# Performance work log

Measured on AMD Instinct MI355X. Metric: run time of the kernel, lower is better.

The kernel has to match this reference:

```python
import jax, jax.numpy as jnp
import numpy as np

T = 128        # number of time points
D = 64         # flattened state dim (bs * z_dim, bs = 1)
H = 256        # hidden width of f-network
HK = 128       # hidden width of kernel network
MAX_IT = 3     # fixed-point iterations (args.max_iterations)


def setup_inputs() -> dict:
    key = jax.random.key(0)
    ks = jax.random.split(key, 6)
    g = lambda k, sh, sc: (jax.random.normal(k, sh, jnp.float32) * sc)
    z0 = jax.random.normal(ks[0], (1, D), jnp.float32)
    t = jnp.linspace(0.0, 1.0, T, dtype=jnp.float32)
    # f: D -> H -> D MLP (the 'func' integrand network)
    W1 = g(ks[1], (D, H), 1.0 / np.sqrt(D)); b1 = jnp.zeros((H,), jnp.float32)
    W2 = g(ks[2], (H, D), 1.0 / np.sqrt(H)); b2 = jnp.zeros((D,), jnp.float32)
    # kernel: (x, s) -> D*D matrix entries (the neural kernel K)
    Wk1 = g(ks[3], (2, HK), 1.0 / np.sqrt(2.0)); bk1 = jnp.zeros((HK,), jnp.float32)
    Wk2 = g(ks[4], (HK, D * D), 1.0 / np.sqrt(HK)); bk2 = jnp.zeros((D * D,), jnp.float32)
    return dict(z0=z0, t=t, W1=W1, b1=b1, W2=W2, b2=b2,
                Wk1=Wk1, bk1=bk1, Wk2=Wk2, bk2=bk2)


def _trapezoid_weights(t):
    """w[i, j]: trapezoid quadrature weight of node j for integral over [t0, t_i]."""
    dt = t[1] - t[0]  # uniform grid
    idx = jnp.arange(T)
    mask = (idx[None, :] <= idx[:, None]).astype(t.dtype)
    w = dt * mask
    w = w.at[(idx, idx)].multiply(0.5)   # halve right endpoint of each row
    w = w.at[:, 0].multiply(0.5)         # halve left endpoint
    w = w.at[0].set(0.0)                 # zero-length integral at t0
    return w


def _solve(z0, t, W1, b1, W2, b2, Wk1, bk1, Wk2, bk2):
    y0 = z0.reshape(-1)                                   # [D], solver flattens batch
    w = _trapezoid_weights(t)                             # [T, T]
    # Neural kernel K(x_i, s_j) -> [D, D], precomputed once on the grid.
    pairs = jnp.stack([jnp.broadcast_to(t[:, None], (T, T)),
                       jnp.broadcast_to(t[None, :], (T, T))], axis=-1)  # [T, T, 2]
    hK = jnp.tanh(pairs @ Wk1 + bk1)                      # [T, T, HK]
    K = (hK @ Wk2 + bk2).reshape(T, T, D, D)              # [T, T, D, D]

    def f(y):  # integrand network, applied over all time points
        return jnp.tanh(y @ W1 + b1) @ W2 + b2            # [T, D]

    def step(y, _):
        # G_i = \int_0^{x_i} K(x_i, s) f(y(s)) ds  (trapezoid on grid)
        G = jnp.einsum('ij,ijde,je->id', w, K, f(y))      # [T, D]
        # y'(x) = G(x)  =>  y_i = y0 + \int_0^{x_i} G(s) ds
        y_new = y0[None, :] + w @ G                       # [T, D]
        return y_new, None

    y_init = jnp.tile(y0[None, :], (T, 1))                # fixed-point initial guess
    y, _ = jax.lax.scan(step, y_init, None, length=MAX_IT)
    return y


def reference(z0, t, W1, b1, W2, b2, Wk1, bk1, Wk2, bk2):
    y = _solve(z0, t, W1, b1, W2, b2, Wk1, bk1, Wk2, bk2)  # [T, D]
    return y[-1].reshape(1, D)  # z[-1]: final state, shape [bs, dim]
```

## Files before the change

kernel.cpp:

```cpp
#include <hip/hip_runtime.h>

#define TT 128
#define DD 64
#define HH 256
#define HKD 128
#define HD (HKD*DD)

static __device__ __forceinline__ float ald(const float* p) {
    return __hip_atomic_load(const_cast<float*>(p), __ATOMIC_RELAXED, __HIP_MEMORY_SCOPE_AGENT);
}
static __device__ __forceinline__ void ast(float* p, float v) {
    __hip_atomic_store(p, v, __ATOMIC_RELAXED, __HIP_MEMORY_SCOPE_AGENT);
}
static __device__ __forceinline__ int aldi(int* p) {
    return __hip_atomic_load(p, __ATOMIC_RELAXED, __HIP_MEMORY_SCOPE_AGENT);
}

__global__ void __launch_bounds__(256)
k_init(const float* __restrict__ z0, const float* __restrict__ t,
       const float* __restrict__ W1, const float* __restrict__ b1,
       const float* __restrict__ W2, const float* __restrict__ b2,
       const float* __restrict__ Wk1, const float* __restrict__ bk1,
       const float* __restrict__ Wk2, const float* __restrict__ bk2,
       float* __restrict__ M0, float* __restrict__ bF0,
       float* __restrict__ Ga, float* __restrict__ Gb, int* m0cnt)
{
    const int b = blockIdx.x, tid = threadIdx.x;
    const int part = tid >> 6, d = tid & 63;
    const float dt = t[1] - t[0];
    __shared__ float red[4][64];
    __shared__ float ys[DD];
    __shared__ float hs[HH];
    __shared__ __attribute__((aligned(16))) float fs[DD];
    __shared__ float Bpart[2][HKD];
    __shared__ float Bs[HKD];

    if (b < 32) {
        if (tid < DD) ys[tid] = z0[tid];
        __syncthreads();
        float acc = b1[tid];
        #pragma unroll 8
        for (int e = 0; e < DD; ++e) acc += ys[e] * W1[e * HH + tid];
        hs[tid] = tanhf(acc);
        __syncthreads();
        {
            float s = 0.f;
            #pragma unroll 8
            for (int h = part * 64; h < part * 64 + 64; ++h) s += hs[h] * W2[h * DD + d];
            red[part][d] = s;
        }
        __syncthreads();
        if (part == 0)
            fs[d] = b2[d] + red[0][d] + red[1][d] + red[2][d] + red[3][d];
        __syncthreads();
        if (b == 0) {
            float s = 0.f;
            #pragma unroll
            for (int e = part * 16; e < part * 16 + 16; ++e) s += bk2[d * DD + e] * fs[e];
            red[part][d] = s;
            __syncthreads();
            if (part == 0)
                ast(&bF0[d], red[0][d] + red[1][d] + red[2][d] + red[3][d]);
        }
        {
            int hd = b * 256 + tid;
            const float* Wrow = Wk2 + (size_t)hd * DD;
            float a = 0.f;
            #pragma unroll
            for (int e = 0; e < DD; e += 8) {
                float4 wa = *(const float4*)(Wrow + e);
                float4 wb = *(const float4*)(Wrow + e + 4);
                float4 fa = *(const float4*)&fs[e];
                float4 fb = *(const float4*)&fs[e + 4];
                a += fa.x*wa.x + fa.y*wa.y + fa.z*wa.z + fa.w*wa.w
                   + fb.x*wb.x + fb.y*wb.y + fb.z*wb.z + fb.w*wb.w;
            }
            ast(&M0[hd], a);
        }
        Gb[b * 256 + tid] = 0.f;
        __syncthreads();
        asm volatile("" ::: "memory");
        if (tid == 0)
            __hip_atomic_fetch_add(m0cnt, 1, __ATOMIC_RELAXED, __HIP_MEMORY_SCOPE_AGENT);
        return;
    }

    const int i = b - 32;
    {
        const int h = tid & 127, half = tid >> 7;
        float bsum = 0.f;
        if (i > 0) {
            const float wk0 = Wk1[h], wk1v = Wk1[HKD + h], bk = bk1[h];
            const float ti = t[i];
            for (int j = half; j <= i; j += 2) {
                float w = dt * ((j == 0 || j == i) ? 0.5f : 1.0f);
                bsum += w * tanhf(ti * wk0 + t[j] * wk1v + bk);
            }
        }
        Bpart[half][h] = bsum;
    }
    __syncthreads();
    if (tid < HKD) Bs[tid] = Bpart[0][tid] + Bpart[1][tid];
    if (tid == 0) { while (aldi(m0cnt) < 32) __builtin_amdgcn_s_sleep(2); }
    asm volatile("" ::: "memory");
    __syncthreads();
    float a = 0.f;
    #pragma unroll 8
    for (int h2 = part * 32; h2 < part * 32 + 32; ++h2)
        a += Bs[h2] * ald(&M0[h2 * DD + d]);
    red[part][d] = a;
    __syncthreads();
    if (part == 0) {
        float g = red[0][d] + red[1][d] + red[2][d] + red[3][d];
        g += dt * (float)i * ald(&bF0[d]);
        Ga[i * DD + d] = (i == 0) ? 0.f : g;
    }
}

__global__ void __launch_bounds__(256)
k_FM(const float* __restrict__ Gin, const float* __restrict__ z0,
     const float* __restrict__ t,
     const float* __restrict__ W1, const float* __restrict__ b1,
     const float* __restrict__ W2, const float* __restrict__ b2,
     const float* __restrict__ bk2, const float* __restrict__ Wk2,
     float* __restrict__ fbuf, float* __restrict__ bFb,
     float* __restrict__ M, int* ftile,
     float* __restrict__ out, int seed_out)
{
    const int b = blockIdx.x, tid = threadIdx.x;
    const int part = tid >> 6, d = tid & 63;
    __shared__ float red[4][64];
    __shared__ float ys[DD];
    __shared__ float hs[HH];
    __shared__ __attribute__((aligned(16))) float Fs[8][DD];
    const float dt = t[1] - t[0];

    if (b < TT) {
        const int j = b;
        float s = 0.f;
        if (j > 0) {
            for (int jp = part; jp <= j; jp += 4) {
                float w = (jp == 0 || jp == j) ? 0.5f : 1.0f;
                s += w * Gin[jp * DD + d];
            }
        }
        red[part][d] = s;
        __syncthreads();
        if (part == 0)
            ys[d] = z0[d] + dt * (red[0][d] + red[1][d] + red[2][d] + red[3][d]);
        __syncthreads();
        float acc = b1[tid];
        #pragma unroll 8
        for (int e = 0; e < DD; ++e) acc += ys[e] * W1[e * HH + tid];
        hs[tid] = tanhf(acc);
        __syncthreads();
        {
            float s2 = 0.f;
            #pragma unroll 8
            for (int h = part * 64; h < part * 64 + 64; ++h) s2 += hs[h] * W2[h * DD + d];
            red[part][d] = s2;
        }
        __syncthreads();
        if (part == 0) {
            float fv = b2[d] + red[0][d] + red[1][d] + red[2][d] + red[3][d];
            ast(&fbuf[j * DD + d], fv);
            ys[d] = fv;
        }
        __syncthreads();
        {
            float s2 = 0.f;
            #pragma unroll
            for (int e = part * 16; e < part * 16 + 16; ++e) s2 += bk2[d * DD + e] * ys[e];
            red[part][d] = s2;
            __syncthreads();
            if (part == 0)
                bFb[j * DD + d] = red[0][d] + red[1][d] + red[2][d] + red[3][d];
        }
        __syncthreads();
        asm volatile("" ::: "memory");
        if (tid == 0)
            __hip_atomic_fetch_add(&ftile[(j >> 3) * 16], 1,
                                   __ATOMIC_RELAXED, __HIP_MEMORY_SCOPE_AGENT);
    }

    const int tilei = b >> 5;
    const int hd = (b & 31) * 256 + tid;
    const int j0 = tilei * 8;
    if (tid == 0) {
        while (aldi(&ftile[tilei * 16]) < 8) __builtin_amdgcn_s_sleep(2);
    }
    asm volatile("" ::: "memory");
    __syncthreads();
    for (int k2 = tid; k2 < 8 * DD; k2 += 256)
        Fs[k2 >> 6][k2 & 63] = ald(&fbuf[j0 * DD + k2]);
    __syncthreads();
    float acc[8] = {0.f,0.f,0.f,0.f,0.f,0.f,0.f,0.f};
    const float* Wrow = Wk2 + (size_t)hd * DD;
    for (int e = 0; e < DD; e += 8) {
        float4 wa = *(const float4*)(Wrow + e);
        float4 wb = *(const float4*)(Wrow + e + 4);
        #pragma unroll
        for (int r = 0; r < 8; ++r) {
            float4 f0 = *(const float4*)&Fs[r][e];
            float4 f1 = *(const float4*)&Fs[r][e + 4];
            acc[r] += f0.x*wa.x + f0.y*wa.y + f0.z*wa.z + f0.w*wa.w
                    + f1.x*wb.x + f1.y*wb.y + f1.z*wb.z + f1.w*wb.w;
        }
    }
    #pragma unroll
    for (int r = 0; r < 8; ++r) M[(size_t)(j0 + r) * HD + hd] = acc[r];

    if (seed_out && b == 128 && tid < DD) out[tid] = z0[tid];
}

__global__ void __launch_bounds__(256)
k_G1a(const float* __restrict__ t, const float* __restrict__ Wk1,
      const float* __restrict__ bk1, const float* __restrict__ M,
      const float* __restrict__ bF,
      float* __restrict__ Gout, float* __restrict__ out, int final_it)
{
    const int itile = blockIdx.x, c = blockIdx.y;
    if (c > 4 * itile + 3) return;
    __shared__ __attribute__((aligned(16))) float As[8 * 256];
    __shared__ float red[4][8][64];
    const int tid = threadIdx.x, part = tid >> 6, d = tid & 63;
    const float dt = t[1] - t[0];

    {
        const int h = tid & 127;
        const int j = 2 * c + (tid >> 7);
        const float wk0 = Wk1[h], wk1v = Wk1[HKD + h], bk = bk1[h];
        const float tj = t[j];
        #pragma unroll
        for (int k = 0; k < 8; ++k) {
            int i = itile * 8 + k;
            float w = (i == 0 || j > i) ? 0.f : dt * ((j == 0 || j == i) ? 0.5f : 1.0f);
            As[k * 256 + tid] = w * tanhf(t[i] * wk0 + tj * wk1v + bk);
        }
    }
    __syncthreads();

    float acc[8] = {0.f,0.f,0.f,0.f,0.f,0.f,0.f,0.f};
    const float* Mp = M + ((size_t)c * 256) * DD + d;
    const int jl0 = part * 64;
    for (int jl = jl0; jl < jl0 + 64; jl += 8) {
        float m0 = Mp[(size_t)(jl + 0) * DD];
        float m1 = Mp[(size_t)(jl + 1) * DD];
        float m2 = Mp[(size_t)(jl + 2) * DD];
        float m3 = Mp[(size_t)(jl + 3) * DD];
        float m4 = Mp[(size_t)(jl + 4) * DD];
        float m5 = Mp[(size_t)(jl + 5) * DD];
        float m6 = Mp[(size_t)(jl + 6) * DD];
        float m7 = Mp[(size_t)(jl + 7) * DD];
        #pragma unroll
        for (int r = 0; r < 8; ++r) {
            float4 a0 = *(const float4*)&As[r * 256 + jl];
            float4 a1 = *(const float4*)&As[r * 256 + jl + 4];
            acc[r] += a0.x*m0 + a0.y*m1 + a0.z*m2 + a0.w*m3
                    + a1.x*m4 + a1.y*m5 + a1.z*m6 + a1.w*m7;
        }
    }
    #pragma unroll
    for (int r = 0; r < 8; ++r) red[part][r][d] = acc[r];
    __syncthreads();
    if (part == 0) {
        if (!final_it) {
            #pragma unroll
            for (int r = 0; r < 8; ++r) {
                float v = red[0][r][d] + red[1][r][d] + red[2][r][d] + red[3][r][d];
                atomicAdd(&Gout[(itile * 8 + r) * DD + d], v);
            }
            if (c == 0) {
                const int i0 = itile * 8;
                float run = 0.5f * bF[d];
                int p = 0;
                for (int r = 0; r < 8; ++r) {
                    int i = i0 + r;
                    if (i == 0) continue;
                    while (p < i - 1) { ++p; run += bF[p * DD + d]; }
                    float term = dt * (run + 0.5f * bF[i * DD + d]);
                    atomicAdd(&Gout[i * DD + d], term);
                }
            }
        } else {
            float vsum = 0.f;
            #pragma unroll
            for (int r = 0; r < 8; ++r) {
                int i = itile * 8 + r;
                float w = (i == 0 || i == TT - 1) ? 0.5f : 1.0f;
                vsum += w * (red[0][r][d] + red[1][r][d] + red[2][r][d] + red[3][r][d]);
            }
            if (c == 0) {
                const int i0 = itile * 8;
                float run = 0.5f * bF[d];
                int p = 0;
                for (int r = 0; r < 8; ++r) {
                    int i = i0 + r;
                    if (i == 0) continue;
                    while (p < i - 1) { ++p; run += bF[p * DD + d]; }
                    float term = dt * (run + 0.5f * bF[i * DD + d]);
                    float w = (i == TT - 1) ? 0.5f : 1.0f;
                    vsum += w * term;
                }
            }
            atomicAdd(&out[d], dt * vsum);
        }
    }
}

extern "C" void kernel_launch(void* const* d_in, const int* in_sizes, int n_in,
                              void* d_out, int out_size, void* d_ws, size_t ws_size,
                              hipStream_t stream) {
    const float* z0  = (const float*)d_in[0];
    const float* t   = (const float*)d_in[1];
    const float* W1  = (const float*)d_in[2];
    const float* b1  = (const float*)d_in[3];
    const float* W2  = (const float*)d_in[4];
    const float* b2  = (const float*)d_in[5];
    const float* Wk1 = (const float*)d_in[6];
    const float* bk1 = (const float*)d_in[7];
    const float* Wk2 = (const float*)d_in[8];
    const float* bk2 = (const float*)d_in[9];
    float* out = (float*)d_out;

    float* ws   = (float*)d_ws;
    float* M    = ws;
    float* M0   = M    + (size_t)TT*HD;
    float* bF0  = M0   + HD;
    float* Ga   = bF0  + DD;
    float* Gb   = Ga   + TT*DD;
    float* fbuf = Gb   + TT*DD;
    float* bFb  = fbuf + TT*DD;
    int*   cnt  = (int*)(bFb + TT*DD);

    int* m0cnt  = cnt;
    int* ftileA = cnt + 16;
    int* ftileB = cnt + 16 + 256;

    hipMemsetAsync(cnt, 0, 528 * sizeof(int), stream);

    k_init<<<160, 256, 0, stream>>>(z0, t, W1, b1, W2, b2, Wk1, bk1, Wk2, bk2,
                                    M0, bF0, Ga, Gb, m0cnt);
    k_FM<<<512, 256, 0, stream>>>(Ga, z0, t, W1, b1, W2, b2, bk2, Wk2,
                                  fbuf, bFb, M, ftileA, out, 0);
    k_G1a<<<dim3(16, 64), 256, 0, stream>>>(t, Wk1, bk1, M, bFb, Gb, out, 0);
    k_FM<<<512, 256, 0, stream>>>(Gb, z0, t, W1, b1, W2, b2, bk2, Wk2,
                                  fbuf, bFb, M, ftileB, out, 1);
    k_G1a<<<dim3(16, 64), 256, 0, stream>>>(t, Wk1, bk1, M, bFb, Gb, out, 1);
}
```

Baseline: 222.5 us.

## Precompute bias prefix integral in k_FM and prefetch M rows into registers

The trapezoid prefix sum of bF, previously recomputed serially per tile by c==0 blocks in k_G1a, is now computed once by the last k_FM block into a new bFint buffer, after waiting on all tile counters. k_G1a then adds a single bFint value per row. It also issues all 64 M loads into registers before building the tanh A tile, so global latency can overlap the tanhf work. The cost is a 32KB shared scan buffer in every k_FM block, which can lower occupancy, a serial 128-step scan in one block, and higher register pressure in k_G1a.

```diff
diff --git a/kernel.cpp b/kernel.cpp
--- a/kernel.cpp
+++ b/kernel.cpp
@@ -124,7 +124,7 @@
      const float* __restrict__ W2, const float* __restrict__ b2,
      const float* __restrict__ bk2, const float* __restrict__ Wk2,
      float* __restrict__ fbuf, float* __restrict__ bFb,
-     float* __restrict__ M, int* ftile,
+     float* __restrict__ M, int* ftile, float* __restrict__ bFint,
      float* __restrict__ out, int seed_out)
 {
     const int b = blockIdx.x, tid = threadIdx.x;
@@ -133,6 +133,7 @@
     __shared__ float ys[DD];
     __shared__ float hs[HH];
     __shared__ __attribute__((aligned(16))) float Fs[8][DD];
+    __shared__ float scanb[TT][DD];
     const float dt = t[1] - t[0];
 
     if (b < TT) {
@@ -174,7 +175,7 @@
             red[part][d] = s2;
             __syncthreads();
             if (part == 0)
-                bFb[j * DD + d] = red[0][d] + red[1][d] + red[2][d] + red[3][d];
+                ast(&bFb[j * DD + d], red[0][d] + red[1][d] + red[2][d] + red[3][d]);
         }
         __syncthreads();
         asm volatile("" ::: "memory");
@@ -211,12 +212,30 @@
     for (int r = 0; r < 8; ++r) M[(size_t)(j0 + r) * HD + hd] = acc[r];
 
     if (seed_out && b == 128 && tid < DD) out[tid] = z0[tid];
+
+    if (b == 511) {
+        if (tid < 16) { while (aldi(&ftile[tid * 16]) < 8) __builtin_amdgcn_s_sleep(2); }
+        asm volatile("" ::: "memory");
+        __syncthreads();
+        for (int idx = tid; idx < TT * DD; idx += 256)
+            scanb[idx >> 6][idx & 63] = ald(&bFb[idx]);
+        __syncthreads();
+        if (tid < DD) {
+            float run = 0.5f * scanb[0][tid];
+            bFint[tid] = 0.f;
+            for (int i = 1; i < TT; ++i) {
+                float v = scanb[i][tid];
+                bFint[i * DD + tid] = dt * (run + 0.5f * v);
+                run += v;
+            }
+        }
+    }
 }
 
 __global__ void __launch_bounds__(256)
 k_G1a(const float* __restrict__ t, const float* __restrict__ Wk1,
       const float* __restrict__ bk1, const float* __restrict__ M,
-      const float* __restrict__ bF,
+      const float* __restrict__ bFint,
       float* __restrict__ Gout, float* __restrict__ out, int final_it)
 {
     const int itile = blockIdx.x, c = blockIdx.y;
@@ -225,6 +244,12 @@
     __shared__ float red[4][8][64];
     const int tid = threadIdx.x, part = tid >> 6, d = tid & 63;
     const float dt = t[1] - t[0];
+    const int jl0 = part * 64;
+
+    const float* Mp = M + ((size_t)c * 256 + jl0) * DD + d;
+    float m[64];
+    #pragma unroll
+    for (int k = 0; k < 64; ++k) m[k] = Mp[(size_t)k * DD];
 
     {
         const int h = tid & 127;
@@ -240,25 +265,18 @@
     }
     __syncthreads();
 
-    float acc[8] = {0.f,0.f,0.f,0.f,0.f,0.f,0.f,0.f};
-    const float* Mp = M + ((size_t)c * 256) * DD + d;
-    const int jl0 = part * 64;
-    for (int jl = jl0; jl < jl0 + 64; jl += 8) {
-        float m0 = Mp[(size_t)(jl + 0) * DD];
-        float m1 = Mp[(size_t)(jl + 1) * DD];
-        float m2 = Mp[(size_t)(jl + 2) * DD];
-        float m3 = Mp[(size_t)(jl + 3) * DD];
-        float m4 = Mp[(size_t)(jl + 4) * DD];
-        float m5 = Mp[(size_t)(jl + 5) * DD];
-        float m6 = Mp[(size_t)(jl + 6) * DD];
-        float m7 = Mp[(size_t)(jl + 7) * DD];
+    float acc[8];
+    const float4* As4 = (const float4*)As;
+    #pragma unroll
+    for (int r = 0; r < 8; ++r) {
+        float s = 0.f;
         #pragma unroll
-        for (int r = 0; r < 8; ++r) {
-            float4 a0 = *(const float4*)&As[r * 256 + jl];
-            float4 a1 = *(const float4*)&As[r * 256 + jl + 4];
-            acc[r] += a0.x*m0 + a0.y*m1 + a0.z*m2 + a0.w*m3
-                    + a1.x*m4 + a1.y*m5 + a1.z*m6 + a1.w*m7;
-        }
+        for (int k4 = 0; k4 < 16; ++k4) {
+            float4 a = As4[r * 64 + (jl0 >> 2) + k4];
+            s += a.x * m[k4 * 4] + a.y * m[k4 * 4 + 1]
+               + a.z * m[k4 * 4 + 2] + a.w * m[k4 * 4 + 3];
+        }
+        acc[r] = s;
     }
     #pragma unroll
     for (int r = 0; r < 8; ++r) red[part][r][d] = acc[r];
@@ -267,20 +285,10 @@
         if (!final_it) {
             #pragma unroll
             for (int r = 0; r < 8; ++r) {
+                int i = itile * 8 + r;
                 float v = red[0][r][d] + red[1][r][d] + red[2][r][d] + red[3][r][d];
-                atomicAdd(&Gout[(itile * 8 + r) * DD + d], v);
-            }
-            if (c == 0) {
-                const int i0 = itile * 8;
-                float run = 0.5f * bF[d];
-                int p = 0;
-                for (int r = 0; r < 8; ++r) {
-                    int i = i0 + r;
-                    if (i == 0) continue;
-                    while (p < i - 1) { ++p; run += bF[p * DD + d]; }
-                    float term = dt * (run + 0.5f * bF[i * DD + d]);
-                    atomicAdd(&Gout[i * DD + d], term);
-                }
+                if (c == 0) v += ald(&bFint[i * DD + d]);
+                atomicAdd(&Gout[i * DD + d], v);
             }
         } else {
             float vsum = 0.f;
@@ -288,20 +296,9 @@
             for (int r = 0; r < 8; ++r) {
                 int i = itile * 8 + r;
                 float w = (i == 0 || i == TT - 1) ? 0.5f : 1.0f;
-                vsum += w * (red[0][r][d] + red[1][r][d] + red[2][r][d] + red[3][r][d]);
-            }
-            if (c == 0) {
-                const int i0 = itile * 8;
-                float run = 0.5f * bF[d];
-                int p = 0;
-                for (int r = 0; r < 8; ++r) {
-                    int i = i0 + r;
-                    if (i == 0) continue;
-                    while (p < i - 1) { ++p; run += bF[p * DD + d]; }
-                    float term = dt * (run + 0.5f * bF[i * DD + d]);
-                    float w = (i == TT - 1) ? 0.5f : 1.0f;
-                    vsum += w * term;
-                }
+                float v = red[0][r][d] + red[1][r][d] + red[2][r][d] + red[3][r][d];
+                if (c == 0) v += ald(&bFint[i * DD + d]);
+                vsum += w * v;
             }
             atomicAdd(&out[d], dt * vsum);
         }
@@ -323,15 +320,16 @@
     const float* bk2 = (const float*)d_in[9];
     float* out = (float*)d_out;
 
-    float* ws   = (float*)d_ws;
-    float* M    = ws;
-    float* M0   = M    + (size_t)TT*HD;
-    float* bF0  = M0   + HD;
-    float* Ga   = bF0  + DD;
-    float* Gb   = Ga   + TT*DD;
-    float* fbuf = Gb   + TT*DD;
-    float* bFb  = fbuf + TT*DD;
-    int*   cnt  = (int*)(bFb + TT*DD);
+    float* ws    = (float*)d_ws;
+    float* M     = ws;
+    float* M0    = M     + (size_t)TT*HD;
+    float* bF0   = M0    + HD;
+    float* Ga    = bF0   + DD;
+    float* Gb    = Ga    + TT*DD;
+    float* fbuf  = Gb    + TT*DD;
+    float* bFb   = fbuf  + TT*DD;
+    float* bFint = bFb   + TT*DD;
+    int*   cnt   = (int*)(bFint + TT*DD);
 
     int* m0cnt  = cnt;
     int* ftileA = cnt + 16;
@@ -342,9 +340,9 @@
     k_init<<<160, 256, 0, stream>>>(z0, t, W1, b1, W2, b2, Wk1, bk1, Wk2, bk2,
                                     M0, bF0, Ga, Gb, m0cnt);
     k_FM<<<512, 256, 0, stream>>>(Ga, z0, t, W1, b1, W2, b2, bk2, Wk2,
-                                  fbuf, bFb, M, ftileA, out, 0);
-    k_G1a<<<dim3(16, 64), 256, 0, stream>>>(t, Wk1, bk1, M, bFb, Gb, out, 0);
+                                  fbuf, bFb, M, ftileA, bFint, out, 0);
+    k_G1a<<<dim3(16, 64), 256, 0, stream>>>(t, Wk1, bk1, M, bFint, Gb, out, 0);
     k_FM<<<512, 256, 0, stream>>>(Gb, z0, t, W1, b1, W2, b2, bk2, Wk2,
-                                  fbuf, bFb, M, ftileB, out, 1);
-    k_G1a<<<dim3(16, 64), 256, 0, stream>>>(t, Wk1, bk1, M, bFb, Gb, out, 1);
-}
+                                  fbuf, bFb, M, ftileB, bFint, out, 1);
+    k_G1a<<<dim3(16, 64), 256, 0, stream>>>(t, Wk1, bk1, M, bFint, Gb, out, 1);
+}
```

Result: faster. 187.3 us (-15.8%).
